# Kernel optimization log

Measured on AMD Instinct MI355X. Metric: run time of the kernel, lower is better.

The kernel has to match this reference:

```python
import jax, jax.numpy as jnp
import numpy as np

N = 32          # objects in the (single) image
P = N * (N - 1) # relation pairs
D = 256         # self.dim
M = 14          # mask_size / pooler resolution
OC = 151        # obj classes
RC = 51         # rel classes
RED = D // 4    # attention gate reduction


def setup_inputs() -> dict:
    key = jax.random.key(0)
    ks = jax.random.split(key, 32)
    # all ordered pairs i != j
    ii, jj = np.meshgrid(np.arange(N), np.arange(N), indexing='ij')
    keep = ii != jj
    rel_pair_idxs = jnp.asarray(np.stack([ii[keep], jj[keep]], 1), jnp.int32)  # [P,2]
    # valid xyxy boxes in an 800x600 image
    x1 = jax.random.uniform(ks[0], (N,)) * 600.0
    y1 = jax.random.uniform(ks[1], (N,)) * 400.0
    w = jax.random.uniform(ks[2], (N,)) * 180.0 + 20.0
    h = jax.random.uniform(ks[3], (N,)) * 180.0 + 20.0
    bboxes = jnp.stack([x1, y1, x1 + w, y1 + h], 1).astype(jnp.float32)
    roi_features = jax.random.normal(ks[4], (N, 4096), jnp.float32)
    predict_logits = jax.random.normal(ks[5], (N, OC), jnp.float32)
    union_features = jax.random.normal(ks[6], (P, D, M, M), jnp.float32)
    s = 0.02
    p = dict(
        roi_features=roi_features, bboxes=bboxes, predict_logits=predict_logits,
        union_features=union_features, rel_pair_idxs=rel_pair_idxs,
        W_emb1=jax.random.normal(ks[7], (4096 + OC + 4, D)) * s, b_emb1=jnp.zeros((D,)),
        W_emb2=jax.random.normal(ks[8], (D, D)) * s, b_emb2=jnp.zeros((D,)),
        # stacked SE-attention gates: 0=sbj, 1=obj, 2=bg
        att_fc1_w=jax.random.normal(ks[9], (3, D, RED)) * s, att_fc1_b=jnp.zeros((3, RED)),
        att_fc2_w=jax.random.normal(ks[10], (3, RED, D)) * s, att_fc2_b=jnp.zeros((3, D)),
        W_c1=jax.random.normal(ks[11], (3 * D, D)) * s, b_c1=jnp.zeros((D,)),
        W_c2=jax.random.normal(ks[12], (D, D)) * s, b_c2=jnp.zeros((D,)),
        W_gcn=jax.random.normal(ks[13], (D, D)) * s, b_gcn=jnp.zeros((D,)),
        W_objp=jax.random.normal(ks[14], (D, OC)) * s, b_objp=jnp.zeros((OC,)),
        W_relp=jax.random.normal(ks[15], (D, RC)) * s, b_relp=jnp.zeros((RC,)),
    )
    return p


def _rect_masks(x0, y0, x1, y1):
    # mask[p, r, c] = 1 iff x0<=r<x1 and y0<=c<y1  (matches torch slice write)
    r = jnp.arange(M, dtype=jnp.float32)
    rm = (r[None, :] >= x0[:, None]) & (r[None, :] < x1[:, None])  # [P,M]
    cm = (r[None, :] >= y0[:, None]) & (r[None, :] < y1[:, None])  # [P,M]
    return (rm[:, :, None] & cm[:, None, :]).astype(jnp.float32)   # [P,M,M]


def _masking(union_features, bboxes, pairs):
    sb = bboxes[pairs[:, 0]]  # [P,4]
    ob = bboxes[pairs[:, 1]]
    ux1 = jnp.minimum(sb[:, 0], ob[:, 0])
    uy1 = jnp.minimum(sb[:, 1], ob[:, 1])
    x = jnp.stack([sb[:, 0], sb[:, 2], ob[:, 0], ob[:, 2]], 1) - ux1[:, None]
    y = jnp.stack([sb[:, 1], sb[:, 3], ob[:, 1], ob[:, 3]], 1) - uy1[:, None]
    xr = M / jnp.maximum(x[:, 1], x[:, 3])
    yr = M / jnp.maximum(y[:, 1], y[:, 3])
    xp = jnp.round(x * xr[:, None])
    yp = jnp.round(y * yr[:, None])
    sm = _rect_masks(xp[:, 0], yp[:, 0], xp[:, 1], yp[:, 1])[:, None]  # [P,1,M,M]
    om = _rect_masks(xp[:, 2], yp[:, 2], xp[:, 3], yp[:, 3])[:, None]
    bm = jnp.clip(1.0 - sm - om, 0.0, 1.0)
    return union_features * sm, union_features * om, union_features * bm


def _att_gate(x, w1, b1, w2, b2):
    # SE-style channel attention gate
    s = x.mean((2, 3))                                        # [P,D]
    g = jax.nn.sigmoid(jax.nn.relu(s @ w1 + b1) @ w2 + b2)    # [P,D]
    return x * g[:, :, None, None]


def _adjacency(pairs):
    o2o = jnp.zeros((N, N)).at[pairs[:, 0], pairs[:, 1]].set(1.0)
    ar = jnp.arange(P)
    o2r = jnp.zeros((N, P)).at[pairs[:, 0], ar].set(1.0).at[pairs[:, 1], ar].set(1.0)
    top = jnp.concatenate([o2o, o2r], 1)                     # [N, N+P]
    bot = jnp.concatenate([o2r.T, jnp.zeros((P, P))], 1)     # [P, N+P]
    adj = jnp.concatenate([top, bot], 0)
    return adj + jnp.eye(N + P)


def reference(roi_features, bboxes, predict_logits, union_features, rel_pair_idxs,
              W_emb1, b_emb1, W_emb2, b_emb2,
              att_fc1_w, att_fc1_b, att_fc2_w, att_fc2_b,
              W_c1, b_c1, W_c2, b_c2, W_gcn, b_gcn,
              W_objp, b_objp, W_relp, b_relp):
    pairs = rel_pair_idxs
    # object embedding
    obj_in = jnp.concatenate([roi_features, predict_logits, bboxes], 1)  # [N,4251]
    obj_feats = jax.nn.relu(obj_in @ W_emb1 + b_emb1) @ W_emb2 + b_emb2  # [N,D]
    # masking + attention gates + global avg pool
    sbj, obj, bg = _masking(union_features, bboxes, pairs)
    sbj = _att_gate(sbj, att_fc1_w[0], att_fc1_b[0], att_fc2_w[0], att_fc2_b[0]).mean((2, 3))
    obj = _att_gate(obj, att_fc1_w[1], att_fc1_b[1], att_fc2_w[1], att_fc2_b[1]).mean((2, 3))
    bg = _att_gate(bg, att_fc1_w[2], att_fc1_b[2], att_fc2_w[2], att_fc2_b[2]).mean((2, 3))
    # relational embedding (compose)
    rel = jnp.concatenate([sbj, obj, bg], 1)                 # [P,3D]
    rel_feats = jax.nn.relu(rel @ W_c1 + b_c1) @ W_c2 + b_c2  # [P,D]
    # GCN over object+relation graph (row-normalized adjacency, residual)
    adj = _adjacency(pairs)
    feats = jnp.concatenate([obj_feats, rel_feats], 0)        # [N+P,D]
    norm_adj = adj / adj.sum(1, keepdims=True)
    gcn_out = jax.nn.relu(norm_adj @ (feats @ W_gcn) + b_gcn) + feats
    obj_dists = gcn_out[:N] @ W_objp + b_objp                 # [N,OC]
    rel_dists = gcn_out[N:] @ W_relp + b_relp                 # [P,RC]
    return obj_dists, rel_dists
```

## Files before the change

kernel.cpp:

```cpp
#include <hip/hip_runtime.h>
#include <cstdint>
#include <cstddef>

#define NOBJ 32
#define NP   992
#define DD   256
#define SP   196
#define OC   151
#define RC   51
#define RED  64
#define KIN  4251
#define CH   128
#define KPC  34

#define OFF_PART   0u
#define OFF_OBJF   1048576u
#define OFF_SALL   1056768u
#define OFF_RELF   1818624u
#define OFF_H      2072576u
#define OFF_W2T    2334720u
#define OFF_WC1T   2400256u
#define OFF_WC2T   2596864u
#define OFF_WGT    2662400u
#define OFF_FC1WT  2727936u
#define OFF_FC2WT  2777088u
#define OFF_WOPT   2826240u
#define OFF_WRPT   2864896u

#define TR_TOT 51712

#define TCH  32
#define NTIL 8
#define TF4  1568

__global__ void __launch_bounds__(256, 5)
k_pre(const float* __restrict__ uf,
      const float* __restrict__ bbox,
      const int* __restrict__ pairs,
      const float* __restrict__ roi,
      const float* __restrict__ logits,
      const float* __restrict__ W1,
      const float* __restrict__ Wop, const float* __restrict__ Wrp,
      float* __restrict__ sAll, float* __restrict__ part,
      float* __restrict__ WopT, float* __restrict__ WrpT) {
  const int b = blockIdx.x, t = threadIdx.x;
  if (b < NP) {
    const int p = b;
    __shared__ __align__(16) float buf[TCH * SP + 28];
    __shared__ __align__(16) float mS[224];
    __shared__ __align__(16) float mO[224];
    __shared__ __align__(16) float mB[224];
    if (t < 224) {
      float sm = 0.f, om = 0.f, bm = 0.f;
      if (t < SP) {
        int si = pairs[2 * p], oi = pairs[2 * p + 1];
        float sx1 = bbox[si * 4 + 0], sy1 = bbox[si * 4 + 1];
        float sx2 = bbox[si * 4 + 2], sy2 = bbox[si * 4 + 3];
        float ox1 = bbox[oi * 4 + 0], oy1 = bbox[oi * 4 + 1];
        float ox2 = bbox[oi * 4 + 2], oy2 = bbox[oi * 4 + 3];
        float ux = fminf(sx1, ox1), uy = fminf(sy1, oy1);
        float xr = 14.f / fmaxf(sx2 - ux, ox2 - ux);
        float yr = 14.f / fmaxf(sy2 - uy, oy2 - uy);
        float xs0 = rintf((sx1 - ux) * xr), xs1 = rintf((sx2 - ux) * xr);
        float xo0 = rintf((ox1 - ux) * xr), xo1 = rintf((ox2 - ux) * xr);
        float ys0 = rintf((sy1 - uy) * yr), ys1 = rintf((sy2 - uy) * yr);
        float yo0 = rintf((oy1 - uy) * yr), yo1 = rintf((oy2 - uy) * yr);
        int a = t / 14, bb = t - a * 14;
        float fa = (float)a, fb = (float)bb;
        sm = (fa >= xs0 && fa < xs1 && fb >= ys0 && fb < ys1) ? 1.f : 0.f;
        om = (fa >= xo0 && fa < xo1 && fb >= yo0 && fb < yo1) ? 1.f : 0.f;
        bm = fminf(fmaxf(1.f - sm - om, 0.f), 1.f);
      }
      mS[t] = sm; mO[t] = om; mB[t] = bm;
    }
    if (t < 28) buf[TCH * SP + t] = 0.f;
    const float4* base4 = (const float4*)(uf + (size_t)p * (DD * SP));
    {
      const float4* src = base4 + t;
      float4* dst = (float4*)buf + t;
      dst[0] = src[0];     dst[256] = src[256];   dst[512] = src[512];
      dst[768] = src[768]; dst[1024] = src[1024]; dst[1280] = src[1280];
      if (t < 32) dst[1536] = src[1536];
    }
    __syncthreads();
    const int cl = t >> 3, o = t & 7;
    const float* row = buf + cl * SP + o * 28;
    const float* msp = mS + o * 28;
    const float* mop = mO + o * 28;
    const float* mbp = mB + o * 28;
    const float inv = 1.f / 196.f;
    float4 s0, s1, s2, s3, s4, s5, s6 = {0.f, 0.f, 0.f, 0.f};
#pragma unroll 1
    for (int ti = 0; ti < NTIL; ++ti) {
      if (ti < NTIL - 1) {
        const float4* src = base4 + (ti + 1) * TF4 + t;
        s0 = src[0];     s1 = src[256];   s2 = src[512];
        s3 = src[768];   s4 = src[1024];  s5 = src[1280];
        if (t < 32) s6 = src[1536];
      }
      float aS = 0.f, aO = 0.f, aB = 0.f;
#pragma unroll
      for (int j = 0; j < 7; ++j) {
        float4 v = *(const float4*)&row[4 * j];
        float4 x = *(const float4*)&msp[4 * j];
        float4 y = *(const float4*)&mop[4 * j];
        float4 z = *(const float4*)&mbp[4 * j];
        aS += v.x * x.x + v.y * x.y + v.z * x.z + v.w * x.w;
        aO += v.x * y.x + v.y * y.y + v.z * y.z + v.w * y.w;
        aB += v.x * z.x + v.y * z.y + v.z * z.z + v.w * z.w;
      }
      aS += __shfl_xor(aS, 1); aS += __shfl_xor(aS, 2); aS += __shfl_xor(aS, 4);
      aO += __shfl_xor(aO, 1); aO += __shfl_xor(aO, 2); aO += __shfl_xor(aO, 4);
      aB += __shfl_xor(aB, 1); aB += __shfl_xor(aB, 2); aB += __shfl_xor(aB, 4);
      const int ch = ti * TCH + cl;
      if (o == 0)      sAll[(size_t)p * 768 + ch]       = aS * inv;
      else if (o == 1) sAll[(size_t)p * 768 + 256 + ch] = aO * inv;
      else if (o == 2) sAll[(size_t)p * 768 + 512 + ch] = aB * inv;
      if (ti < NTIL - 1) {
        __syncthreads();
        float4* dst = (float4*)buf + t;
        dst[0] = s0;     dst[256] = s1;   dst[512] = s2;
        dst[768] = s3;   dst[1024] = s4;  dst[1280] = s5;
        if (t < 32) dst[1536] = s6;
        __syncthreads();
      }
    }
  } else if (b < NP + CH) {
    const int chunk = b - NP;
    int k0 = chunk * KPC;
    int k1 = k0 + KPC; if (k1 > KIN) k1 = KIN;
    float acc[NOBJ];
#pragma unroll
    for (int i = 0; i < NOBJ; ++i) acc[i] = 0.f;
#pragma unroll 2
    for (int k = k0; k < k1; ++k) {
      float w = W1[(size_t)k * DD + t];
      const float* xp; int stride;
      if (k < 4096)            { xp = roi    + k;               stride = 4096; }
      else if (k < 4096 + OC)  { xp = logits + (k - 4096);      stride = OC;   }
      else                     { xp = bbox   + (k - 4096 - OC); stride = 4;    }
#pragma unroll
      for (int i = 0; i < NOBJ; ++i) { acc[i] += xp[0] * w; xp += stride; }
    }
    float* pout = part + (size_t)chunk * (NOBJ * DD) + t;
#pragma unroll
    for (int i = 0; i < NOBJ; ++i) pout[i * DD] = acc[i];
  } else {
    for (int o = (b - NP - CH) * 256 + t; o < TR_TOT; o += 64 * 256) {
      float v; float* dst;
      if (o < 38656) { int q = o;         v = Wop[(q & 255) * OC + (q >> 8)]; dst = WopT + q; }
      else           { int q = o - 38656; v = Wrp[(q & 255) * RC + (q >> 8)]; dst = WrpT + q; }
      *dst = v;
    }
  }
}

__global__ void __launch_bounds__(256, 4)
k_mid2(const float* __restrict__ sAll,
       const float* __restrict__ f1w, const float* __restrict__ f1b,
       const float* __restrict__ f2w, const float* __restrict__ f2b,
       const float* __restrict__ Wc1, const float* __restrict__ bc1,
       const float* __restrict__ Wc2, const float* __restrict__ bc2,
       const float* __restrict__ Wg,
       const float* __restrict__ part, const float* __restrict__ b1,
       const float* __restrict__ W2,  const float* __restrict__ b2,
       float* __restrict__ relf, float* __restrict__ objf,
       float* __restrict__ H) {
  const int b = blockIdx.x, t = threadIdx.x;
  __shared__ __align__(16) float sg[4][768];
  __shared__ __align__(16) float ha[4][192];
  __shared__ __align__(16) float h2[4][256];
  __shared__ __align__(16) float hob[256];
  __shared__ __align__(16) float eob[256];
  if (b < NP / 4) {
    const int w = t >> 6, l = t & 63;
    const int r = b * 4 + w;
    {
      const float4* src = (const float4*)(sAll + (size_t)r * 768);
      float4* dst = (float4*)&sg[w][0];
      dst[l] = src[l]; dst[64 + l] = src[64 + l]; dst[128 + l] = src[128 + l];
    }
    __syncthreads();
    {
      float a0 = 0.f, a1 = 0.f, a2 = 0.f;
      const float* w0 = f1w + l;
      const float* w1 = f1w + 16384 + l;
      const float* w2 = f1w + 32768 + l;
#pragma unroll 4
      for (int d4 = 0; d4 < 64; ++d4) {
        float4 x0 = *((const float4*)&sg[w][0]   + d4);
        float4 x1 = *((const float4*)&sg[w][256] + d4);
        float4 x2 = *((const float4*)&sg[w][512] + d4);
        int d = 4 * d4;
        a0 += x0.x * w0[d * 64] + x0.y * w0[(d + 1) * 64] +
              x0.z * w0[(d + 2) * 64] + x0.w * w0[(d + 3) * 64];
        a1 += x1.x * w1[d * 64] + x1.y * w1[(d + 1) * 64] +
              x1.z * w1[(d + 2) * 64] + x1.w * w1[(d + 3) * 64];
        a2 += x2.x * w2[d * 64] + x2.y * w2[(d + 1) * 64] +
              x2.z * w2[(d + 2) * 64] + x2.w * w2[(d + 3) * 64];
      }
      ha[w][l]       = fmaxf(a0 + f1b[l], 0.f);
      ha[w][64 + l]  = fmaxf(a1 + f1b[64 + l], 0.f);
      ha[w][128 + l] = fmaxf(a2 + f1b[128 + l], 0.f);
    }
    __syncthreads();
#pragma unroll
    for (int br = 0; br < 3; ++br) {
      float ax = 0.f, ay = 0.f, az = 0.f, aw = 0.f;
      const float4* wp = (const float4*)(f2w + br * 16384) + l;
#pragma unroll 8
      for (int red = 0; red < 64; ++red) {
        float x = ha[w][br * 64 + red];
        float4 wv = wp[red * 64];
        ax += x * wv.x; ay += x * wv.y; az += x * wv.z; aw += x * wv.w;
      }
      float4 bb = *((const float4*)(f2b + br * 256) + l);
      float4 sv = *((float4*)&sg[w][br * 256] + l);
      sv.x *= 1.f / (1.f + expf(-(ax + bb.x)));
      sv.y *= 1.f / (1.f + expf(-(ay + bb.y)));
      sv.z *= 1.f / (1.f + expf(-(az + bb.z)));
      sv.w *= 1.f / (1.f + expf(-(aw + bb.w)));
      *((float4*)&sg[w][br * 256] + l) = sv;
    }
    __syncthreads();
    {
      float ax = 0.f, ay = 0.f, az = 0.f, aw = 0.f;
      const float4* wp = (const float4*)Wc1 + l;
#pragma unroll 4
      for (int k4 = 0; k4 < 192; ++k4) {
        float4 x = *((const float4*)&sg[w][0] + k4);
        int k = 4 * k4;
        float4 v0 = wp[(size_t)k * 64], v1 = wp[(size_t)(k + 1) * 64];
        float4 v2 = wp[(size_t)(k + 2) * 64], v3 = wp[(size_t)(k + 3) * 64];
        ax += x.x * v0.x + x.y * v1.x + x.z * v2.x + x.w * v3.x;
        ay += x.x * v0.y + x.y * v1.y + x.z * v2.y + x.w * v3.y;
        az += x.x * v0.z + x.y * v1.z + x.z * v2.z + x.w * v3.z;
        aw += x.x * v0.w + x.y * v1.w + x.z * v2.w + x.w * v3.w;
      }
      float4 bb = *((const float4*)bc1 + l);
      float4 hv;
      hv.x = fmaxf(ax + bb.x, 0.f); hv.y = fmaxf(ay + bb.y, 0.f);
      hv.z = fmaxf(az + bb.z, 0.f); hv.w = fmaxf(aw + bb.w, 0.f);
      *((float4*)&h2[w][0] + l) = hv;
    }
    __syncthreads();
    {
      float ax = 0.f, ay = 0.f, az = 0.f, aw = 0.f;
      const float4* wp = (const float4*)Wc2 + l;
#pragma unroll 4
      for (int k4 = 0; k4 < 64; ++k4) {
        float4 x = *((const float4*)&h2[w][0] + k4);
        int k = 4 * k4;
        float4 v0 = wp[k * 64], v1 = wp[(k + 1) * 64];
        float4 v2 = wp[(k + 2) * 64], v3 = wp[(k + 3) * 64];
        ax += x.x * v0.x + x.y * v1.x + x.z * v2.x + x.w * v3.x;
        ay += x.x * v0.y + x.y * v1.y + x.z * v2.y + x.w * v3.y;
        az += x.x * v0.z + x.y * v1.z + x.z * v2.z + x.w * v3.z;
        aw += x.x * v0.w + x.y * v1.w + x.z * v2.w + x.w * v3.w;
      }
      float4 bb = *((const float4*)bc2 + l);
      float4 v; v.x = ax + bb.x; v.y = ay + bb.y; v.z = az + bb.z; v.w = aw + bb.w;
      *(float4*)(relf + (size_t)r * DD + 4 * l) = v;
      *((float4*)&sg[w][0] + l) = v;
    }
    __syncthreads();
    {
      float ax = 0.f, ay = 0.f, az = 0.f, aw = 0.f;
      const float4* wp = (const float4*)Wg + l;
#pragma unroll 4
      for (int k4 = 0; k4 < 64; ++k4) {
        float4 x = *((const float4*)&sg[w][0] + k4);
        int k = 4 * k4;
        float4 v0 = wp[k * 64], v1 = wp[(k + 1) * 64];
        float4 v2 = wp[(k + 2) * 64], v3 = wp[(k + 3) * 64];
        ax += x.x * v0.x + x.y * v1.x + x.z * v2.x + x.w * v3.x;
        ay += x.x * v0.y + x.y * v1.y + x.z * v2.y + x.w * v3.y;
        az += x.x * v0.z + x.y * v1.z + x.z * v2.z + x.w * v3.z;
        aw += x.x * v0.w + x.y * v1.w + x.z * v2.w + x.w * v3.w;
      }
      float4 v; v.x = ax; v.y = ay; v.z = az; v.w = aw;
      *(float4*)(H + (size_t)(NOBJ + r) * DD + 4 * l) = v;
    }
  } else {
    const int i = b - NP / 4;
    float s[8];
#pragma unroll
    for (int u = 0; u < 8; ++u) s[u] = 0.f;
#pragma unroll
    for (int c0 = 0; c0 < CH; c0 += 8) {
#pragma unroll
      for (int u = 0; u < 8; ++u)
        s[u] += part[(size_t)(c0 + u) * (NOBJ * DD) + i * DD + t];
    }
    float tot = ((s[0] + s[1]) + (s[2] + s[3])) + ((s[4] + s[5]) + (s[6] + s[7]));
    hob[t] = fmaxf(tot + b1[t], 0.f);
    __syncthreads();
    {
      float a = 0.f;
#pragma unroll 4
      for (int k4 = 0; k4 < 64; ++k4) {
        float4 hv = *((const float4*)hob + k4);
        int k = 4 * k4;
        a += hv.x * W2[k * 256 + t]       + hv.y * W2[(k + 1) * 256 + t]
           + hv.z * W2[(k + 2) * 256 + t] + hv.w * W2[(k + 3) * 256 + t];
      }
      float v = a + b2[t];
      objf[i * DD + t] = v;
      eob[t] = v;
    }
    __syncthreads();
    {
      float a = 0.f;
#pragma unroll 4
      for (int k4 = 0; k4 < 64; ++k4) {
        float4 ev = *((const float4*)eob + k4);
        int k = 4 * k4;
        a += ev.x * Wg[k * 256 + t]       + ev.y * Wg[(k + 1) * 256 + t]
           + ev.z * Wg[(k + 2) * 256 + t] + ev.w * Wg[(k + 3) * 256 + t];
      }
      H[(size_t)i * DD + t] = a;
    }
  }
}

__global__ void __launch_bounds__(1024, 1)
k_heads(const float* __restrict__ H, const float* __restrict__ objf,
        const float* __restrict__ relf, const int* __restrict__ pairs,
        const float* __restrict__ bg,
        const float* __restrict__ WopT, const float* __restrict__ bop,
        const float* __restrict__ WrpT, const float* __restrict__ brp,
        float* __restrict__ out) {
  const int b = blockIdx.x, t = threadIdx.x;
  const int p = t >> 8, tt = t & 255;
  if (b < NP / 4) {
    __shared__ __align__(16) float gr[4][DD];
    __shared__ float red[4][4][64];
    const int r = b * 4 + p;
    int si = pairs[2 * r], oi = pairs[2 * r + 1];
    float hsum = H[si * DD + tt] + H[oi * DD + tt] + H[(size_t)(NOBJ + r) * DD + tt];
    gr[p][tt] = fmaxf(hsum * (1.f / 3.f) + bg[tt], 0.f) + relf[(size_t)r * DD + tt];
    __syncthreads();
    const int q = tt >> 6, c = tt & 63;
    float a = 0.f;
    if (c < RC) {
      const float4* w4 = (const float4*)(WrpT + c * 256 + q * 64);
#pragma unroll
      for (int j = 0; j < 16; ++j) {
        float4 wv = w4[j];
        float4 gv = *(const float4*)&gr[p][q * 64 + 4 * j];
        a += gv.x * wv.x + gv.y * wv.y + gv.z * wv.z + gv.w * wv.w;
      }
    }
    red[p][q][c] = a;
    __syncthreads();
    if (tt < RC)
      out[NOBJ * OC + (size_t)r * RC + tt] =
          red[p][0][tt] + red[p][1][tt] + red[p][2][tt] + red[p][3][tt] + brp[tt];
  } else {
    const int i = b - NP / 4;
    const int slice = p;
    __shared__ int2 pr[NP];
    __shared__ float red2[4][DD];
    __shared__ __align__(16) float gro[DD];
    const int2* p2 = (const int2*)pairs;
    for (int r = t; r < NP; r += 1024) pr[r] = p2[r];
    __syncthreads();
    float acc = 0.f;
    if (slice == 0) {
#pragma unroll 8
      for (int j = 0; j < NOBJ; ++j) acc += H[j * DD + tt];
    }
    const int rbeg = slice * 248;
#pragma unroll 8
    for (int r = rbeg; r < rbeg + 248; ++r) {
      int2 q = pr[r];
      float v = H[(size_t)(NOBJ + r) * DD + tt];
      if (q.x == i || q.y == i) acc += v;
    }
    red2[slice][tt] = acc;
    __syncthreads();
    if (t < DD) {
      float pre = (red2[0][t] + red2[1][t] + red2[2][t] + red2[3][t]) * (1.f / 94.f);
      gro[t] = fmaxf(pre + bg[t], 0.f) + objf[i * DD + t];
    }
    __syncthreads();
    float hsum = 0.f;
    if (tt < OC) {
      const float4* w4 = (const float4*)(WopT + tt * 256 + slice * 64);
#pragma unroll
      for (int j = 0; j < 16; ++j) {
        float4 wv = w4[j];
        float4 gv = *(const float4*)&gro[slice * 64 + 4 * j];
        hsum += gv.x * wv.x + gv.y * wv.y + gv.z * wv.z + gv.w * wv.w;
      }
    }
    red2[slice][tt] = hsum;
    __syncthreads();
    if (t < OC)
      out[i * OC + t] = red2[0][t] + red2[1][t] + red2[2][t] + red2[3][t] + bop[t];
  }
}

extern "C" void kernel_launch(void* const* d_in, const int* in_sizes, int n_in,
                              void* d_out, int out_size, void* d_ws, size_t ws_size,
                              hipStream_t stream) {
  const float* roi   = (const float*)d_in[0];
  const float* bbox  = (const float*)d_in[1];
  const float* logit = (const float*)d_in[2];
  const float* uf    = (const float*)d_in[3];
  const int*   pairs = (const int*)d_in[4];
  const float* W1    = (const float*)d_in[5];
  const float* b1    = (const float*)d_in[6];
  const float* W2    = (const float*)d_in[7];
  const float* b2    = (const float*)d_in[8];
  const float* fc1w  = (const float*)d_in[9];
  const float* fc1b  = (const float*)d_in[10];
  const float* fc2w  = (const float*)d_in[11];
  const float* fc2b  = (const float*)d_in[12];
  const float* Wc1   = (const float*)d_in[13];
  const float* bc1   = (const float*)d_in[14];
  const float* Wc2   = (const float*)d_in[15];
  const float* bc2   = (const float*)d_in[16];
  const float* Wg    = (const float*)d_in[17];
  const float* bg    = (const float*)d_in[18];
  const float* Wop   = (const float*)d_in[19];
  const float* bop   = (const float*)d_in[20];
  const float* Wrp   = (const float*)d_in[21];
  const float* brp   = (const float*)d_in[22];

  float* ws    = (float*)d_ws;
  float* part  = ws + OFF_PART;
  float* objf  = ws + OFF_OBJF;
  float* sAll  = ws + OFF_SALL;
  float* relf  = ws + OFF_RELF;
  float* Hbuf  = ws + OFF_H;
  float* WopT  = ws + OFF_WOPT;
  float* WrpT  = ws + OFF_WRPT;
  float* out   = (float*)d_out;

  k_pre<<<NP + CH + 64, 256, 0, stream>>>(uf, bbox, pairs, roi, logit, W1,
                                          Wop, Wrp, sAll, part, WopT, WrpT);
  k_mid2<<<NP / 4 + NOBJ, 256, 0, stream>>>(sAll, fc1w, fc1b, fc2w, fc2b,
                                            Wc1, bc1, Wc2, bc2, Wg,
                                            part, b1, W2, b2, relf, objf, Hbuf);
  k_heads<<<NP / 4 + NOBJ, 1024, 0, stream>>>(Hbuf, objf, relf, pairs, bg,
                                              WopT, bop, WrpT, brp, out);
}
```

Measured before the change: 514.3 us.

## Process two relation rows per block so each weight load serves both

The relation MLP stage in k_mid2 now handles two pairs per block instead of four. Each thread owns one output column and accumulates both rows at once, so every scalar weight load is reused across two rows. Before, each wave did its own row with float4 weight loads, so each block reread the weights once per row. The change doubles the block count and halves per-row weight traffic, but drops float4 weight loads and leaves 64 threads idle in the fc1 step.

```diff
diff --git a/kernel.cpp b/kernel.cpp
--- a/kernel.cpp
+++ b/kernel.cpp
@@ -18,12 +18,6 @@
 #define OFF_SALL   1056768u
 #define OFF_RELF   1818624u
 #define OFF_H      2072576u
-#define OFF_W2T    2334720u
-#define OFF_WC1T   2400256u
-#define OFF_WC2T   2596864u
-#define OFF_WGT    2662400u
-#define OFF_FC1WT  2727936u
-#define OFF_FC2WT  2777088u
 #define OFF_WOPT   2826240u
 #define OFF_WRPT   2864896u
 
@@ -155,6 +149,24 @@
   }
 }
 
+#define DOT8(WP, STR, X0, X1, K, A0, A1)                                      \
+  { float w0v = (WP)[(size_t)((K) + 0) * (STR)],                              \
+          w1v = (WP)[(size_t)((K) + 1) * (STR)],                              \
+          w2v = (WP)[(size_t)((K) + 2) * (STR)],                              \
+          w3v = (WP)[(size_t)((K) + 3) * (STR)],                              \
+          w4v = (WP)[(size_t)((K) + 4) * (STR)],                              \
+          w5v = (WP)[(size_t)((K) + 5) * (STR)],                              \
+          w6v = (WP)[(size_t)((K) + 6) * (STR)],                              \
+          w7v = (WP)[(size_t)((K) + 7) * (STR)];                              \
+    float4 xa0 = *(const float4*)&(X0)[(K)];                                  \
+    float4 xb0 = *(const float4*)&(X0)[(K) + 4];                              \
+    float4 xa1 = *(const float4*)&(X1)[(K)];                                  \
+    float4 xb1 = *(const float4*)&(X1)[(K) + 4];                              \
+    A0 += xa0.x * w0v + xa0.y * w1v + xa0.z * w2v + xa0.w * w3v               \
+        + xb0.x * w4v + xb0.y * w5v + xb0.z * w6v + xb0.w * w7v;              \
+    A1 += xa1.x * w0v + xa1.y * w1v + xa1.z * w2v + xa1.w * w3v               \
+        + xb1.x * w4v + xb1.y * w5v + xb1.z * w6v + xb1.w * w7v; }
+
 __global__ void __launch_bounds__(256, 4)
 k_mid2(const float* __restrict__ sAll,
        const float* __restrict__ f1w, const float* __restrict__ f1b,
@@ -167,122 +179,80 @@
        float* __restrict__ relf, float* __restrict__ objf,
        float* __restrict__ H) {
   const int b = blockIdx.x, t = threadIdx.x;
-  __shared__ __align__(16) float sg[4][768];
-  __shared__ __align__(16) float ha[4][192];
-  __shared__ __align__(16) float h2[4][256];
+  __shared__ __align__(16) float sg[2][768];
+  __shared__ __align__(16) float ha[2][192];
+  __shared__ __align__(16) float h2[2][256];
+  __shared__ __align__(16) float rf[2][256];
   __shared__ __align__(16) float hob[256];
   __shared__ __align__(16) float eob[256];
-  if (b < NP / 4) {
-    const int w = t >> 6, l = t & 63;
-    const int r = b * 4 + w;
-    {
-      const float4* src = (const float4*)(sAll + (size_t)r * 768);
-      float4* dst = (float4*)&sg[w][0];
-      dst[l] = src[l]; dst[64 + l] = src[64 + l]; dst[128 + l] = src[128 + l];
-    }
-    __syncthreads();
-    {
-      float a0 = 0.f, a1 = 0.f, a2 = 0.f;
-      const float* w0 = f1w + l;
-      const float* w1 = f1w + 16384 + l;
-      const float* w2 = f1w + 32768 + l;
-#pragma unroll 4
-      for (int d4 = 0; d4 < 64; ++d4) {
-        float4 x0 = *((const float4*)&sg[w][0]   + d4);
-        float4 x1 = *((const float4*)&sg[w][256] + d4);
-        float4 x2 = *((const float4*)&sg[w][512] + d4);
-        int d = 4 * d4;
-        a0 += x0.x * w0[d * 64] + x0.y * w0[(d + 1) * 64] +
-              x0.z * w0[(d + 2) * 64] + x0.w * w0[(d + 3) * 64];
-        a1 += x1.x * w1[d * 64] + x1.y * w1[(d + 1) * 64] +
-              x1.z * w1[(d + 2) * 64] + x1.w * w1[(d + 3) * 64];
-        a2 += x2.x * w2[d * 64] + x2.y * w2[(d + 1) * 64] +
-              x2.z * w2[(d + 2) * 64] + x2.w * w2[(d + 3) * 64];
-      }
-      ha[w][l]       = fmaxf(a0 + f1b[l], 0.f);
-      ha[w][64 + l]  = fmaxf(a1 + f1b[64 + l], 0.f);
-      ha[w][128 + l] = fmaxf(a2 + f1b[128 + l], 0.f);
+  if (b < NP / 2) {
+    const int r0 = b * 2;
+    const int tt = t;
+    for (int j = t; j < 384; j += 256) {
+      int pr = j / 192, off = j - pr * 192;
+      ((float4*)&sg[pr][0])[off] =
+          ((const float4*)(sAll + (size_t)(r0 + pr) * 768))[off];
+    }
+    __syncthreads();
+    if (tt < 192) {
+      const int br = tt >> 6;
+      const float* wp = f1w + br * 16384 + (tt & 63);
+      const float* x0 = &sg[0][br * 256];
+      const float* x1 = &sg[1][br * 256];
+      float a0 = 0.f, a1 = 0.f;
+      for (int k8 = 0; k8 < 32; ++k8) DOT8(wp, 64, x0, x1, k8 * 8, a0, a1)
+      float bb = f1b[tt];
+      ha[0][tt] = fmaxf(a0 + bb, 0.f);
+      ha[1][tt] = fmaxf(a1 + bb, 0.f);
     }
     __syncthreads();
 #pragma unroll
     for (int br = 0; br < 3; ++br) {
-      float ax = 0.f, ay = 0.f, az = 0.f, aw = 0.f;
-      const float4* wp = (const float4*)(f2w + br * 16384) + l;
-#pragma unroll 8
-      for (int red = 0; red < 64; ++red) {
-        float x = ha[w][br * 64 + red];
-        float4 wv = wp[red * 64];
-        ax += x * wv.x; ay += x * wv.y; az += x * wv.z; aw += x * wv.w;
-      }
-      float4 bb = *((const float4*)(f2b + br * 256) + l);
-      float4 sv = *((float4*)&sg[w][br * 256] + l);
-      sv.x *= 1.f / (1.f + expf(-(ax + bb.x)));
-      sv.y *= 1.f / (1.f + expf(-(ay + bb.y)));
-      sv.z *= 1.f / (1.f + expf(-(az + bb.z)));
-      sv.w *= 1.f / (1.f + expf(-(aw + bb.w)));
-      *((float4*)&sg[w][br * 256] + l) = sv;
-    }
-    __syncthreads();
-    {
-      float ax = 0.f, ay = 0.f, az = 0.f, aw = 0.f;
-      const float4* wp = (const float4*)Wc1 + l;
-#pragma unroll 4
-      for (int k4 = 0; k4 < 192; ++k4) {
-        float4 x = *((const float4*)&sg[w][0] + k4);
-        int k = 4 * k4;
-        float4 v0 = wp[(size_t)k * 64], v1 = wp[(size_t)(k + 1) * 64];
-        float4 v2 = wp[(size_t)(k + 2) * 64], v3 = wp[(size_t)(k + 3) * 64];
-        ax += x.x * v0.x + x.y * v1.x + x.z * v2.x + x.w * v3.x;
-        ay += x.x * v0.y + x.y * v1.y + x.z * v2.y + x.w * v3.y;
-        az += x.x * v0.z + x.y * v1.z + x.z * v2.z + x.w * v3.z;
-        aw += x.x * v0.w + x.y * v1.w + x.z * v2.w + x.w * v3.w;
-      }
-      float4 bb = *((const float4*)bc1 + l);
-      float4 hv;
-      hv.x = fmaxf(ax + bb.x, 0.f); hv.y = fmaxf(ay + bb.y, 0.f);
-      hv.z = fmaxf(az + bb.z, 0.f); hv.w = fmaxf(aw + bb.w, 0.f);
-      *((float4*)&h2[w][0] + l) = hv;
-    }
-    __syncthreads();
-    {
-      float ax = 0.f, ay = 0.f, az = 0.f, aw = 0.f;
-      const float4* wp = (const float4*)Wc2 + l;
-#pragma unroll 4
-      for (int k4 = 0; k4 < 64; ++k4) {
-        float4 x = *((const float4*)&h2[w][0] + k4);
-        int k = 4 * k4;
-        float4 v0 = wp[k * 64], v1 = wp[(k + 1) * 64];
-        float4 v2 = wp[(k + 2) * 64], v3 = wp[(k + 3) * 64];
-        ax += x.x * v0.x + x.y * v1.x + x.z * v2.x + x.w * v3.x;
-        ay += x.x * v0.y + x.y * v1.y + x.z * v2.y + x.w * v3.y;
-        az += x.x * v0.z + x.y * v1.z + x.z * v2.z + x.w * v3.z;
-        aw += x.x * v0.w + x.y * v1.w + x.z * v2.w + x.w * v3.w;
-      }
-      float4 bb = *((const float4*)bc2 + l);
-      float4 v; v.x = ax + bb.x; v.y = ay + bb.y; v.z = az + bb.z; v.w = aw + bb.w;
-      *(float4*)(relf + (size_t)r * DD + 4 * l) = v;
-      *((float4*)&sg[w][0] + l) = v;
-    }
-    __syncthreads();
-    {
-      float ax = 0.f, ay = 0.f, az = 0.f, aw = 0.f;
-      const float4* wp = (const float4*)Wg + l;
-#pragma unroll 4
-      for (int k4 = 0; k4 < 64; ++k4) {
-        float4 x = *((const float4*)&sg[w][0] + k4);
-        int k = 4 * k4;
-        float4 v0 = wp[k * 64], v1 = wp[(k + 1) * 64];
-        float4 v2 = wp[(k + 2) * 64], v3 = wp[(k + 3) * 64];
-        ax += x.x * v0.x + x.y * v1.x + x.z * v2.x + x.w * v3.x;
-        ay += x.x * v0.y + x.y * v1.y + x.z * v2.y + x.w * v3.y;
-        az += x.x * v0.z + x.y * v1.z + x.z * v2.z + x.w * v3.z;
-        aw += x.x * v0.w + x.y * v1.w + x.z * v2.w + x.w * v3.w;
-      }
-      float4 v; v.x = ax; v.y = ay; v.z = az; v.w = aw;
-      *(float4*)(H + (size_t)(NOBJ + r) * DD + 4 * l) = v;
+      const float* wp = f2w + br * 16384 + tt;
+      const float* x0 = &ha[0][br * 64];
+      const float* x1 = &ha[1][br * 64];
+      float a0 = 0.f, a1 = 0.f;
+      for (int r8 = 0; r8 < 8; ++r8) DOT8(wp, 256, x0, x1, r8 * 8, a0, a1)
+      float bb = f2b[br * 256 + tt];
+      sg[0][br * 256 + tt] *= 1.f / (1.f + expf(-(a0 + bb)));
+      sg[1][br * 256 + tt] *= 1.f / (1.f + expf(-(a1 + bb)));
+    }
+    __syncthreads();
+    {
+      const float* wp = Wc1 + tt;
+      const float* x0 = &sg[0][0];
+      const float* x1 = &sg[1][0];
+      float a0 = 0.f, a1 = 0.f;
+      for (int k8 = 0; k8 < 96; ++k8) DOT8(wp, 256, x0, x1, k8 * 8, a0, a1)
+      float bb = bc1[tt];
+      h2[0][tt] = fmaxf(a0 + bb, 0.f);
+      h2[1][tt] = fmaxf(a1 + bb, 0.f);
+    }
+    __syncthreads();
+    {
+      const float* wp = Wc2 + tt;
+      const float* x0 = &h2[0][0];
+      const float* x1 = &h2[1][0];
+      float a0 = 0.f, a1 = 0.f;
+      for (int k8 = 0; k8 < 32; ++k8) DOT8(wp, 256, x0, x1, k8 * 8, a0, a1)
+      float bb = bc2[tt];
+      float v0 = a0 + bb, v1 = a1 + bb;
+      relf[(size_t)r0 * DD + tt] = v0;
+      relf[(size_t)(r0 + 1) * DD + tt] = v1;
+      rf[0][tt] = v0; rf[1][tt] = v1;
+    }
+    __syncthreads();
+    {
+      const float* wp = Wg + tt;
+      const float* x0 = &rf[0][0];
+      const float* x1 = &rf[1][0];
+      float a0 = 0.f, a1 = 0.f;
+      for (int k8 = 0; k8 < 32; ++k8) DOT8(wp, 256, x0, x1, k8 * 8, a0, a1)
+      H[(size_t)(NOBJ + r0) * DD + tt] = a0;
+      H[(size_t)(NOBJ + r0 + 1) * DD + tt] = a1;
     }
   } else {
-    const int i = b - NP / 4;
+    const int i = b - NP / 2;
     float s[8];
 #pragma unroll
     for (int u = 0; u < 8; ++u) s[u] = 0.f;
@@ -440,7 +410,7 @@
 
   k_pre<<<NP + CH + 64, 256, 0, stream>>>(uf, bbox, pairs, roi, logit, W1,
                                           Wop, Wrp, sAll, part, WopT, WrpT);
-  k_mid2<<<NP / 4 + NOBJ, 256, 0, stream>>>(sAll, fc1w, fc1b, fc2w, fc2b,
+  k_mid2<<<NP / 2 + NOBJ, 256, 0, stream>>>(sAll, fc1w, fc1b, fc2w, fc2b,
                                             Wc1, bc1, Wc2, bc2, Wg,
                                             part, b1, W2, b2, relf, objf, Hbuf);
   k_heads<<<NP / 4 + NOBJ, 1024, 0, stream>>>(Hbuf, objf, relf, pairs, bg,
```

Result: faster. 454.5 us (-11.6%).
